# Performance work log

Hardware: AMD Instinct MI355X
Metric: run time of the kernel (lower is better)

Reference implementation:

```python
import jax, jax.numpy as jnp
import numpy as np

N_NODES = 100000
N_EDGES = 3200000
D_FEAT = 128
N_LAYERS = 2

def setup_inputs() -> dict:
    key = jax.random.key(0)
    k1, k2, k3, k4 = jax.random.split(key, 4)
    x = jax.random.normal(k1, (N_NODES, D_FEAT), dtype=jnp.float32)
    edge_row = jax.random.randint(k2, (N_EDGES,), 0, N_NODES)  # destination (spmm output row)
    edge_col = jax.random.randint(k3, (N_EDGES,), 0, N_NODES)  # source node
    edge_vals = jax.random.uniform(k4, (N_EDGES,), dtype=jnp.float32)
    scalars = jnp.ones((N_LAYERS,), dtype=jnp.float32)  # per-layer learned scalar (init ones)
    return {"x": x, "edge_row": edge_row, "edge_col": edge_col,
            "edge_vals": edge_vals, "scalars": scalars}

def reference(x, edge_row, edge_col, edge_vals, scalars):
    # ScalarSGC forward with dropout p=0 (identity). Same adjacency each layer.
    for l in range(N_LAYERS):
        h = scalars[l] * x                      # scalar * x
        msg = edge_vals[:, None] * h[edge_col]  # [E, D] gather + scale
        agg = jax.ops.segment_sum(msg, edge_row, num_segments=N_NODES)  # spmm
        x = jax.nn.elu(agg)
    return x
```

## Files before the change

kernel.cpp:

```cpp
#include <hip/hip_runtime.h>
#include <math.h>
#include <stdint.h>


#define D_FEAT 128
#define D2     64
#define SCAN_TILE 1024

#define PB 256
#define PT 1024
#define RB_BITS 7
#define ROWS_PER_BUCKET 128
#define COL_BITS 17
#define SEG_SHIFT 14

__device__ __forceinline__ uint32_t f2bf(float f) {
    uint32_t u = __float_as_uint(f);
    return (u + 0x7FFFu + ((u >> 16) & 1u)) >> 16;
}
__device__ __forceinline__ float bf_lo(uint32_t w) { return __uint_as_float(w << 16); }
__device__ __forceinline__ float bf_hi(uint32_t w) { return __uint_as_float(w & 0xFFFF0000u); }

__global__ void convert_kernel(const float2* __restrict__ xin, uint32_t* __restrict__ xbf, int n2) {
    int i = blockIdx.x * blockDim.x + threadIdx.x;
    if (i < n2) {
        float2 f = xin[i];
        xbf[i] = f2bf(f.x) | (f2bf(f.y) << 16);
    }
}

__global__ __launch_bounds__(PT) void coarse_count_kernel(const int* __restrict__ row,
                                                          int* __restrict__ cnt,
                                                          int E, int nbuck) {
    __shared__ int hist[1024];
    const int t = threadIdx.x;
    hist[t] = 0;
    __syncthreads();
    const int stride = PB * PT;
    for (int i = blockIdx.x * PT + t; i < E; i += stride)
        atomicAdd(&hist[row[i] >> RB_BITS], 1);
    __syncthreads();
    if (t < nbuck) cnt[t * PB + blockIdx.x] = hist[t];
}

__global__ __launch_bounds__(SCAN_TILE) void scan1_kernel(const int* __restrict__ counts,
                                                          int* __restrict__ excl,
                                                          int* __restrict__ tileSums, int n) {
    __shared__ int wsum[16];
    const int tid  = threadIdx.x;
    const int lane = tid & 63;
    const int wave = tid >> 6;
    const int i    = blockIdx.x * SCAN_TILE + tid;

    int v = (i < n) ? counts[i] : 0;
    int incl = v;
    #pragma unroll
    for (int off = 1; off < 64; off <<= 1) {
        int t = __shfl_up(incl, off, 64);
        if (lane >= off) incl += t;
    }
    if (lane == 63) wsum[wave] = incl;
    __syncthreads();
    if (wave == 0) {
        int s = (lane < 16) ? wsum[lane] : 0;
        #pragma unroll
        for (int off = 1; off < 16; off <<= 1) {
            int t = __shfl_up(s, off, 64);
            if (lane >= off) s += t;
        }
        if (lane < 16) wsum[lane] = s;
    }
    __syncthreads();
    int wbase = (wave == 0) ? 0 : wsum[wave - 1];
    if (i < n) excl[i] = wbase + (incl - v);
    if (tid == 0) tileSums[blockIdx.x] = wsum[15];
}

__global__ __launch_bounds__(1024) void scan2_kernel(const int* __restrict__ tileSums,
                                                     int* __restrict__ tileBase,
                                                     int* __restrict__ total_out, int nb) {
    __shared__ int buf[1024];
    const int tid = threadIdx.x;
    int v = (tid < nb) ? tileSums[tid] : 0;
    buf[tid] = v;
    __syncthreads();
    #pragma unroll
    for (int off = 1; off < 1024; off <<= 1) {
        int t = (tid >= off) ? buf[tid - off] : 0;
        __syncthreads();
        buf[tid] += t;
        __syncthreads();
    }
    if (tid < nb) tileBase[tid] = buf[tid] - v;
    if (tid == nb - 1) *total_out = buf[tid];
}

__global__ __launch_bounds__(PT) void partition_kernel(const int* __restrict__ row,
                                                       const int* __restrict__ col,
                                                       const float* __restrict__ val,
                                                       const int* __restrict__ cnt,
                                                       const int* __restrict__ tileBase,
                                                       int2* __restrict__ pack2,
                                                       int E, int nbuck) {
    __shared__ int cur[1024];
    const int t = threadIdx.x;
    if (t < nbuck) {
        int idx = t * PB + blockIdx.x;
        cur[t] = cnt[idx] + tileBase[idx >> 10];
    }
    __syncthreads();
    const int stride = PB * PT;
    for (int i = blockIdx.x * PT + t; i < E; i += stride) {
        int r = row[i];
        int pos = atomicAdd(&cur[r >> RB_BITS], 1);
        pack2[pos] = make_int2(col[i] | ((r & (ROWS_PER_BUCKET - 1)) << COL_BITS),
                               __float_as_int(val[i]));
    }
}

__global__ __launch_bounds__(1024) void fine_sort_kernel(const int* __restrict__ cnt,
                                                         const int* __restrict__ tileBase,
                                                         const int2* __restrict__ pack2,
                                                         int2* __restrict__ pack,
                                                         int* __restrict__ offsets,
                                                         int E, int N, int nbuck) {
    __shared__ int bins[1024];
    const int b = blockIdx.x;
    const int t = threadIdx.x;
    const int start = cnt[b << 8] + tileBase[b >> 2];
    const int end   = (b == nbuck - 1) ? E : (cnt[(b + 1) << 8] + tileBase[(b + 1) >> 2]);
    const int n  = end - start;

    bins[t] = 0;
    __syncthreads();

    for (int i = t; i < n; i += 1024) {
        int key = pack2[start + i].x;
        int lr  = ((unsigned)key) >> COL_BITS;
        int seg = (key & ((1 << COL_BITS) - 1)) >> SEG_SHIFT;
        atomicAdd(&bins[(lr << 3) | seg], 1);
    }
    __syncthreads();

    int v = bins[t];
    for (int off = 1; off < 1024; off <<= 1) {
        int tv = (t >= off) ? bins[t - off] : 0;
        __syncthreads();
        bins[t] += tv;
        __syncthreads();
    }
    bins[t] -= v;
    __syncthreads();

    if (t < ROWS_PER_BUCKET) {
        int r = (b << RB_BITS) + t;
        if (r < N) offsets[r] = start + bins[t << 3];
    }
    if (b == 0 && t == 0) offsets[N] = E;
    __syncthreads();

    for (int i = t; i < n; i += 1024) {
        int2 w = pack2[start + i];
        int lr  = ((unsigned)w.x) >> COL_BITS;
        int col = w.x & ((1 << COL_BITS) - 1);
        int p = atomicAdd(&bins[(lr << 3) | (col >> SEG_SHIFT)], 1);
        pack[start + p] = make_int2(col, w.y);
    }
}

template <int OUT_BF16>
__global__ __launch_bounds__(256) void spmm_elu_kernel(
    const int* __restrict__ offsets, const int2* __restrict__ pack,
    const uint32_t* __restrict__ xin, void* __restrict__ xout,
    const float* __restrict__ scalars, int layer, int N) {
    const int tid = threadIdx.x;
    const int grp = tid >> 4;
    const int sub = tid & 15;
    const int r   = blockIdx.x * 16 + grp;

    int e = 0, end = 0;
    if (r < N) { e = offsets[r]; end = offsets[r + 1]; }

    const uint4* __restrict__ xin4 = (const uint4*)xin;

    float a[8];
    #pragma unroll
    for (int k = 0; k < 8; ++k) a[k] = 0.f;

    #define FMA8(W, V)                                                     \
        a[0] += (V) * bf_lo((W).x); a[1] += (V) * bf_hi((W).x);            \
        a[2] += (V) * bf_lo((W).y); a[3] += (V) * bf_hi((W).y);            \
        a[4] += (V) * bf_lo((W).z); a[5] += (V) * bf_hi((W).z);            \
        a[6] += (V) * bf_lo((W).w); a[7] += (V) * bf_hi((W).w);

    for (; e + 4 <= end; e += 4) {
        int2 p0 = pack[e], p1 = pack[e + 1], p2 = pack[e + 2], p3 = pack[e + 3];
        uint4 w0 = xin4[(((uint32_t)p0.x) << 4) + sub];
        uint4 w1 = xin4[(((uint32_t)p1.x) << 4) + sub];
        uint4 w2 = xin4[(((uint32_t)p2.x) << 4) + sub];
        uint4 w3 = xin4[(((uint32_t)p3.x) << 4) + sub];
        FMA8(w0, __int_as_float(p0.y));
        FMA8(w1, __int_as_float(p1.y));
        FMA8(w2, __int_as_float(p2.y));
        FMA8(w3, __int_as_float(p3.y));
    }
    for (; e < end; ++e) {
        int2 p = pack[e];
        uint4 w = xin4[(((uint32_t)p.x) << 4) + sub];
        FMA8(w, __int_as_float(p.y));
    }
    #undef FMA8

    const float s = scalars[layer];
    #pragma unroll
    for (int k = 0; k < 8; ++k) {
        float x = a[k] * s;
        a[k] = (x > 0.f) ? x : (expf(x) - 1.f);
    }

    if (r < N) {
        if (OUT_BF16) {
            uint4 o;
            o.x = f2bf(a[0]) | (f2bf(a[1]) << 16);
            o.y = f2bf(a[2]) | (f2bf(a[3]) << 16);
            o.z = f2bf(a[4]) | (f2bf(a[5]) << 16);
            o.w = f2bf(a[6]) | (f2bf(a[7]) << 16);
            ((uint4*)xout)[(size_t)r * 16 + sub] = o;
        } else {
            ((float4*)xout)[(size_t)r * 32 + sub * 2]     = make_float4(a[0], a[1], a[2], a[3]);
            ((float4*)xout)[(size_t)r * 32 + sub * 2 + 1] = make_float4(a[4], a[5], a[6], a[7]);
        }
    }
}

extern "C" void kernel_launch(void* const* d_in, const int* in_sizes, int n_in,
                              void* d_out, int out_size, void* d_ws, size_t ws_size,
                              hipStream_t stream) {
    const float* x         = (const float*)d_in[0];
    const int*   edge_row  = (const int*)d_in[1];
    const int*   edge_col  = (const int*)d_in[2];
    const float* edge_vals = (const float*)d_in[3];
    const float* scalars   = (const float*)d_in[4];

    const int N = in_sizes[0] / D_FEAT;
    const int E = in_sizes[1];
    const int nbuck = (N + ROWS_PER_BUCKET - 1) >> RB_BITS;
    const int M = nbuck * PB;
    const int NB = (M + SCAN_TILE - 1) / SCAN_TILE;

    char*  ws  = (char*)d_ws;
    size_t off = 0;
    auto alloc = [&](size_t bytes) -> void* {
        off = (off + 255) & ~(size_t)255;
        void* p = ws + off;
        off += bytes;
        return p;
    };
    int*      offsets  = (int*)alloc((size_t)(N + 1) * sizeof(int));
    int*      cnt      = (int*)alloc((size_t)(M + 1) * sizeof(int));
    int*      tileSums = (int*)alloc((size_t)NB * sizeof(int));
    int*      tileBase = (int*)alloc((size_t)NB * sizeof(int));
    int2*     pack2    = (int2*)alloc((size_t)E * sizeof(int2));
    int2*     pack     = (int2*)alloc((size_t)E * sizeof(int2));
    uint32_t* xbf      = (uint32_t*)alloc((size_t)N * D2 * sizeof(uint32_t));
    uint32_t* hbf      = (uint32_t*)pack2;
    (void)ws_size;

    convert_kernel<<<(N * D2 + 255) / 256, 256, 0, stream>>>((const float2*)x, xbf, N * D2);
    coarse_count_kernel<<<PB, PT, 0, stream>>>(edge_row, cnt, E, nbuck);
    scan1_kernel<<<NB, SCAN_TILE, 0, stream>>>(cnt, cnt, tileSums, M);
    scan2_kernel<<<1, 1024, 0, stream>>>(tileSums, tileBase, cnt + M, NB);
    partition_kernel<<<PB, PT, 0, stream>>>(edge_row, edge_col, edge_vals, cnt, tileBase,
                                            pack2, E, nbuck);
    fine_sort_kernel<<<nbuck, 1024, 0, stream>>>(cnt, tileBase, pack2, pack, offsets, E, N, nbuck);

    const int nblk = (N + 15) / 16;
    spmm_elu_kernel<1><<<nblk, 256, 0, stream>>>(offsets, pack, xbf, hbf, scalars, 0, N);
    spmm_elu_kernel<0><<<nblk, 256, 0, stream>>>(offsets, pack, hbf, (void*)d_out, scalars, 1, N);
}
```

Before: 432.2 us.

## Replace two-pass bucket sort with direct global-atomic CSR build

Swaps the coarse bucket partition plus fine in-block sort for a simpler CSR construction: per-row global atomic counts, a scan, then a scatter that places each edge with a global atomicAdd on its row cursor. This removes one full pass over the edge array and the intermediate pack2 buffer. The cost is heavy global atomic traffic on 3.2M edges and the loss of column ordering within rows, which reduces gather locality in the SpMM and makes edge order nondeterministic.

```diff
diff --git a/kernel.cpp b/kernel.cpp
--- a/kernel.cpp
+++ b/kernel.cpp
@@ -6,13 +6,6 @@
 #define D_FEAT 128
 #define D2     64
 #define SCAN_TILE 1024
-
-#define PB 256
-#define PT 1024
-#define RB_BITS 7
-#define ROWS_PER_BUCKET 128
-#define COL_BITS 17
-#define SEG_SHIFT 14
 
 __device__ __forceinline__ uint32_t f2bf(float f) {
     uint32_t u = __float_as_uint(f);
@@ -29,18 +22,10 @@
     }
 }
 
-__global__ __launch_bounds__(PT) void coarse_count_kernel(const int* __restrict__ row,
-                                                          int* __restrict__ cnt,
-                                                          int E, int nbuck) {
-    __shared__ int hist[1024];
-    const int t = threadIdx.x;
-    hist[t] = 0;
-    __syncthreads();
-    const int stride = PB * PT;
-    for (int i = blockIdx.x * PT + t; i < E; i += stride)
-        atomicAdd(&hist[row[i] >> RB_BITS], 1);
-    __syncthreads();
-    if (t < nbuck) cnt[t * PB + blockIdx.x] = hist[t];
+__global__ __launch_bounds__(256) void count_kernel(const int* __restrict__ row,
+                                                    int* __restrict__ cnt, int E) {
+    int i = blockIdx.x * 256 + threadIdx.x;
+    if (i < E) atomicAdd(&cnt[row[i]], 1);
 }
 
 __global__ __launch_bounds__(SCAN_TILE) void scan1_kernel(const int* __restrict__ counts,
@@ -95,76 +80,29 @@
     if (tid == nb - 1) *total_out = buf[tid];
 }
 
-__global__ __launch_bounds__(PT) void partition_kernel(const int* __restrict__ row,
-                                                       const int* __restrict__ col,
-                                                       const float* __restrict__ val,
-                                                       const int* __restrict__ cnt,
+__global__ __launch_bounds__(256) void add_base_kernel(const int* __restrict__ excl,
                                                        const int* __restrict__ tileBase,
-                                                       int2* __restrict__ pack2,
-                                                       int E, int nbuck) {
-    __shared__ int cur[1024];
-    const int t = threadIdx.x;
-    if (t < nbuck) {
-        int idx = t * PB + blockIdx.x;
-        cur[t] = cnt[idx] + tileBase[idx >> 10];
-    }
-    __syncthreads();
-    const int stride = PB * PT;
-    for (int i = blockIdx.x * PT + t; i < E; i += stride) {
+                                                       int* __restrict__ offsets,
+                                                       int* __restrict__ cur, int N, int E) {
+    int i = blockIdx.x * 256 + threadIdx.x;
+    if (i < N) {
+        int v = excl[i] + tileBase[i >> 10];
+        offsets[i] = v;
+        cur[i] = v;
+    }
+    if (i == 0) offsets[N] = E;
+}
+
+__global__ __launch_bounds__(256) void scatter_kernel(const int* __restrict__ row,
+                                                      const int* __restrict__ col,
+                                                      const float* __restrict__ val,
+                                                      int* __restrict__ cur,
+                                                      int2* __restrict__ pack, int E) {
+    int i = blockIdx.x * 256 + threadIdx.x;
+    if (i < E) {
         int r = row[i];
-        int pos = atomicAdd(&cur[r >> RB_BITS], 1);
-        pack2[pos] = make_int2(col[i] | ((r & (ROWS_PER_BUCKET - 1)) << COL_BITS),
-                               __float_as_int(val[i]));
-    }
-}
-
-__global__ __launch_bounds__(1024) void fine_sort_kernel(const int* __restrict__ cnt,
-                                                         const int* __restrict__ tileBase,
-                                                         const int2* __restrict__ pack2,
-                                                         int2* __restrict__ pack,
-                                                         int* __restrict__ offsets,
-                                                         int E, int N, int nbuck) {
-    __shared__ int bins[1024];
-    const int b = blockIdx.x;
-    const int t = threadIdx.x;
-    const int start = cnt[b << 8] + tileBase[b >> 2];
-    const int end   = (b == nbuck - 1) ? E : (cnt[(b + 1) << 8] + tileBase[(b + 1) >> 2]);
-    const int n  = end - start;
-
-    bins[t] = 0;
-    __syncthreads();
-
-    for (int i = t; i < n; i += 1024) {
-        int key = pack2[start + i].x;
-        int lr  = ((unsigned)key) >> COL_BITS;
-        int seg = (key & ((1 << COL_BITS) - 1)) >> SEG_SHIFT;
-        atomicAdd(&bins[(lr << 3) | seg], 1);
-    }
-    __syncthreads();
-
-    int v = bins[t];
-    for (int off = 1; off < 1024; off <<= 1) {
-        int tv = (t >= off) ? bins[t - off] : 0;
-        __syncthreads();
-        bins[t] += tv;
-        __syncthreads();
-    }
-    bins[t] -= v;
-    __syncthreads();
-
-    if (t < ROWS_PER_BUCKET) {
-        int r = (b << RB_BITS) + t;
-        if (r < N) offsets[r] = start + bins[t << 3];
-    }
-    if (b == 0 && t == 0) offsets[N] = E;
-    __syncthreads();
-
-    for (int i = t; i < n; i += 1024) {
-        int2 w = pack2[start + i];
-        int lr  = ((unsigned)w.x) >> COL_BITS;
-        int col = w.x & ((1 << COL_BITS) - 1);
-        int p = atomicAdd(&bins[(lr << 3) | (col >> SEG_SHIFT)], 1);
-        pack[start + p] = make_int2(col, w.y);
+        int pos = atomicAdd(&cur[r], 1);
+        pack[pos] = make_int2(col[i], __float_as_int(val[i]));
     }
 }
 
@@ -244,9 +182,7 @@
 
     const int N = in_sizes[0] / D_FEAT;
     const int E = in_sizes[1];
-    const int nbuck = (N + ROWS_PER_BUCKET - 1) >> RB_BITS;
-    const int M = nbuck * PB;
-    const int NB = (M + SCAN_TILE - 1) / SCAN_TILE;
+    const int NB = (N + SCAN_TILE - 1) / SCAN_TILE;
 
     char*  ws  = (char*)d_ws;
     size_t off = 0;
@@ -257,22 +193,23 @@
         return p;
     };
     int*      offsets  = (int*)alloc((size_t)(N + 1) * sizeof(int));
-    int*      cnt      = (int*)alloc((size_t)(M + 1) * sizeof(int));
-    int*      tileSums = (int*)alloc((size_t)NB * sizeof(int));
+    int*      cnt      = (int*)alloc((size_t)N * sizeof(int));
+    int*      cur      = (int*)alloc((size_t)N * sizeof(int));
+    int*      tileSums = (int*)alloc((size_t)(NB + 1) * sizeof(int));
     int*      tileBase = (int*)alloc((size_t)NB * sizeof(int));
-    int2*     pack2    = (int2*)alloc((size_t)E * sizeof(int2));
     int2*     pack     = (int2*)alloc((size_t)E * sizeof(int2));
     uint32_t* xbf      = (uint32_t*)alloc((size_t)N * D2 * sizeof(uint32_t));
-    uint32_t* hbf      = (uint32_t*)pack2;
+    uint32_t* hbf      = (uint32_t*)alloc((size_t)N * D2 * sizeof(uint32_t));
     (void)ws_size;
 
+    hipMemsetAsync(cnt, 0, (size_t)N * sizeof(int), stream);
     convert_kernel<<<(N * D2 + 255) / 256, 256, 0, stream>>>((const float2*)x, xbf, N * D2);
-    coarse_count_kernel<<<PB, PT, 0, stream>>>(edge_row, cnt, E, nbuck);
-    scan1_kernel<<<NB, SCAN_TILE, 0, stream>>>(cnt, cnt, tileSums, M);
-    scan2_kernel<<<1, 1024, 0, stream>>>(tileSums, tileBase, cnt + M, NB);
-    partition_kernel<<<PB, PT, 0, stream>>>(edge_row, edge_col, edge_vals, cnt, tileBase,
-                                            pack2, E, nbuck);
-    fine_sort_kernel<<<nbuck, 1024, 0, stream>>>(cnt, tileBase, pack2, pack, offsets, E, N, nbuck);
+    count_kernel<<<(E + 255) / 256, 256, 0, stream>>>(edge_row, cnt, E);
+    scan1_kernel<<<NB, SCAN_TILE, 0, stream>>>(cnt, cnt, tileSums, N);
+    scan2_kernel<<<1, 1024, 0, stream>>>(tileSums, tileBase, tileSums + NB, NB);
+    add_base_kernel<<<(N + 255) / 256, 256, 0, stream>>>(cnt, tileBase, offsets, cur, N, E);
+    scatter_kernel<<<(E + 255) / 256, 256, 0, stream>>>(edge_row, edge_col, edge_vals,
+                                                        cur, pack, E);
 
     const int nblk = (N + 15) / 16;
     spmm_elu_kernel<1><<<nblk, 256, 0, stream>>>(offsets, pack, xbf, hbf, scalars, 0, N);
```

Result: slower. 670.3 us (+55.1%).
